# Optimization experiments

Hardware: AMD Instinct MI355X
Metric: run time of the kernel (lower is better)

Reference implementation:

```python
import jax, jax.numpy as jnp
import numpy as np

D_MODEL = 1024
D_FF = 4096
NUM_EXPERTS = 8
TOP_K = 2
BATCH = 2
SEQ = 2048


def setup_inputs() -> dict:
    key = jax.random.key(0)
    ks = jax.random.split(key, 6)
    s_in = 1.0 / np.sqrt(D_MODEL)
    s_ff = 1.0 / np.sqrt(D_FF)
    return {
        "x": jax.random.normal(ks[0], (BATCH, SEQ, D_MODEL), dtype=jnp.float32),
        "gate_w": jax.random.normal(ks[1], (D_MODEL, NUM_EXPERTS), dtype=jnp.float32) * s_in,
        "w1": jax.random.normal(ks[2], (NUM_EXPERTS, D_MODEL, D_FF), dtype=jnp.float32) * s_in,
        "b1": jnp.zeros((NUM_EXPERTS, D_FF), dtype=jnp.float32),
        "w2": jax.random.normal(ks[3], (NUM_EXPERTS, D_FF, D_MODEL), dtype=jnp.float32) * s_ff,
        "b2": jnp.zeros((NUM_EXPERTS, D_MODEL), dtype=jnp.float32),
    }


def reference(x, gate_w, w1, b1, w2, b2):
    B, S, D = x.shape
    T = B * S
    # Router: logits -> softmax -> top-k -> renormalize selected weights
    router_logits = jnp.einsum("bsd,de->bse", x, gate_w)  # [B,S,E]
    probs = jax.nn.softmax(router_logits, axis=-1)
    top_k_weights, top_k_indices = jax.lax.top_k(probs, TOP_K)  # [B,S,K]
    top_k_weights = top_k_weights / jnp.sum(top_k_weights, axis=-1, keepdims=True)

    x_flat = x.reshape(T, D)
    # per-token, per-expert combine weight: sum over k of weight * (idx==e) -> [T,E]
    one_hot = jax.nn.one_hot(top_k_indices.reshape(T, TOP_K), NUM_EXPERTS, dtype=x.dtype)
    combine = jnp.einsum("tke,tk->te", one_hot, top_k_weights.reshape(T, TOP_K))

    # Dense grouped-GEMM over all experts (same math as masked gather/scatter loop,
    # since combine weight is zero for unselected experts)
    h = jnp.maximum(jnp.einsum("td,edf->etf", x_flat, w1) + b1[:, None, :], 0.0)  # [E,T,F]
    y = jnp.einsum("etf,efd->etd", h, w2) + b2[:, None, :]  # [E,T,D]
    out_flat = jnp.einsum("etd,te->td", y, combine)  # [T,D]
    output = out_flat.reshape(B, S, D)
    return output, router_logits, top_k_indices, top_k_weights
```

## Files before the change

kernel.cpp:

```cpp
#include <hip/hip_runtime.h>
#include <cstdint>
#include <cstddef>


#define D_MODEL 1024
#define D_FF    4096
#define NEXP    8
#define TOKENS  4096
#define SLOTS   8192
#define SLOTSP  9216

typedef __bf16 bf16x8 __attribute__((ext_vector_type(8)));
typedef float  f32x4  __attribute__((ext_vector_type(4)));

static __device__ __forceinline__ unsigned short f2bf(float f) {
  unsigned int u = __float_as_uint(f);
  u += 0x7fffu + ((u >> 16) & 1u);
  return (unsigned short)(u >> 16);
}

static __device__ __forceinline__ void async_ld16(const void* g, void* l) {
  __builtin_amdgcn_global_load_lds(
      (const __attribute__((address_space(1))) void*)g,
      (__attribute__((address_space(3))) void*)l, 16, 0, 0);
}


__global__ void init_kernel(int* __restrict__ tok_list) {
  const int g = blockIdx.x * 256 + threadIdx.x;
  if (g < SLOTSP) tok_list[g] = -1;
}

__global__ __launch_bounds__(256) void router_kernel(
    const float* __restrict__ x, const float* __restrict__ gw,
    float* __restrict__ out_logits, float* __restrict__ out_idx,
    float* __restrict__ out_w)
{
  const int w = threadIdx.x >> 6, lane = threadIdx.x & 63;
  const int t = blockIdx.x * 4 + w;
  float p[NEXP];
#pragma unroll
  for (int e = 0; e < NEXP; ++e) p[e] = 0.f;
  const float* xr = x + (size_t)t * D_MODEL;
#pragma unroll 4
  for (int i = 0; i < D_MODEL / 64; ++i) {
    const int d = i * 64 + lane;
    const float xv = xr[d];
    const float* g = gw + (size_t)d * NEXP;
#pragma unroll
    for (int e = 0; e < NEXP; ++e) p[e] += xv * g[e];
  }
#pragma unroll
  for (int e = 0; e < NEXP; ++e) {
#pragma unroll
    for (int s = 1; s < 64; s <<= 1) p[e] += __shfl_xor(p[e], s, 64);
  }
  if (lane == 0) {
    int i0 = 0;
#pragma unroll
    for (int e = 1; e < NEXP; ++e) if (p[e] > p[i0]) i0 = e;
    int i1 = (i0 == 0) ? 1 : 0;
#pragma unroll
    for (int e = 0; e < NEXP; ++e)
      if (e != i0 && p[e] > p[i1]) i1 = e;
    const float w0 = 1.f / (1.f + __expf(p[i1] - p[i0]));
#pragma unroll
    for (int e = 0; e < NEXP; ++e) out_logits[(size_t)t * NEXP + e] = p[e];
    out_idx[t * 2 + 0] = (float)i0;
    out_idx[t * 2 + 1] = (float)i1;
    out_w[t * 2 + 0] = w0;
    out_w[t * 2 + 1] = 1.f - w0;
  }
}

__global__ __launch_bounds__(256) void count_offsets_kernel(
    const float* __restrict__ out_idx, int* __restrict__ wsI)
{
  __shared__ int hist[NEXP];
  const int tid = threadIdx.x;
  if (tid < NEXP) hist[tid] = 0;
  if (tid < NEXP) wsI[8 + tid] = 0;
  __syncthreads();
  int c[NEXP];
#pragma unroll
  for (int e = 0; e < NEXP; ++e) c[e] = 0;
  for (int p = tid * 32; p < tid * 32 + 32; ++p) c[(int)out_idx[p]]++;
#pragma unroll
  for (int e = 0; e < NEXP; ++e) if (c[e]) atomicAdd(&hist[e], c[e]);
  __syncthreads();
  if (tid == 0) {
    int s = 0, nb = 0;
    for (int e = 0; e < NEXP; ++e) {
      wsI[16 + e] = s;
      const int nblk = (hist[e] + 127) >> 7;
      for (int j = 0; j < nblk; ++j) {
        wsI[32 + nb] = e;
        wsI[128 + nb] = s + j * 128;
        ++nb;
      }
      s += nblk << 7;
    }
    wsI[16 + NEXP] = s;
    wsI[25] = nb;
  }
}

__global__ void scatter_kernel(const float* __restrict__ out_idx,
                               int* __restrict__ cursor,
                               const int* __restrict__ po,
                               int* __restrict__ pair_slot,
                               int* __restrict__ tok_list)
{
  const int p = blockIdx.x * 256 + threadIdx.x;
  const int lane = threadIdx.x & 63;
  const int e = (int)out_idx[p];
  int pos = 0;
#pragma unroll
  for (int e8 = 0; e8 < NEXP; ++e8) {
    const unsigned long long m = __ballot(e == e8);
    if (m) {
      const int leader = __ffsll((long long)m) - 1;
      int base = 0;
      if (lane == leader) base = atomicAdd(&cursor[e8], (int)__popcll(m));
      base = __shfl(base, leader, 64);
      if (e == e8)
        pos = po[e8] + base +
              (int)__popcll(m & ((1ull << lane) - 1ull));
    }
  }
  tok_list[pos] = p >> 1;
  pair_slot[p] = pos;
}

__global__ __launch_bounds__(256) void gather_cvt(
    const float* __restrict__ x, const int* __restrict__ tok_list,
    unsigned short* __restrict__ xg)
{
  const int gid = blockIdx.x * 256 + threadIdx.x;
  const int row = gid >> 7, seg = gid & 127;
  const int tok = tok_list[row];
  if (tok < 0) return;
  const float* src = x + (size_t)tok * D_MODEL + seg * 8;
  const float4 a = *(const float4*)(src);
  const float4 b = *(const float4*)(src + 4);
  ushort4 lo = make_ushort4(f2bf(a.x), f2bf(a.y), f2bf(a.z), f2bf(a.w));
  ushort4 hi = make_ushort4(f2bf(b.x), f2bf(b.y), f2bf(b.z), f2bf(b.w));
  unsigned short* d = xg + (size_t)row * D_MODEL + seg * 8;
  *(ushort4*)(d) = lo;
  *(ushort4*)(d + 4) = hi;
}

__global__ __launch_bounds__(256) void transpose_cvt(
    const float* __restrict__ src, unsigned short* __restrict__ dst,
    int K, int N)
{
  const int e = blockIdx.z;
  const int n0 = blockIdx.x * 64;
  const int k0 = blockIdx.y * 64;
  __shared__ float t[64][65];
  const int c4 = (threadIdx.x & 15) * 4;
  const int r  = threadIdx.x >> 4;
  const float* s = src + (size_t)e * K * N + (size_t)k0 * N + n0;
#pragma unroll
  for (int i = 0; i < 4; ++i) {
    const float4 v = *(const float4*)(s + (size_t)(r + 16 * i) * N + c4);
    t[r + 16 * i][c4 + 0] = v.x;
    t[r + 16 * i][c4 + 1] = v.y;
    t[r + 16 * i][c4 + 2] = v.z;
    t[r + 16 * i][c4 + 3] = v.w;
  }
  __syncthreads();
  unsigned short* d = dst + (size_t)e * N * K + (size_t)n0 * K + k0;
#pragma unroll
  for (int i = 0; i < 4; ++i) {
    const int n = r + 16 * i;
    ushort4 v;
    v.x = f2bf(t[c4 + 0][n]);
    v.y = f2bf(t[c4 + 1][n]);
    v.z = f2bf(t[c4 + 2][n]);
    v.w = f2bf(t[c4 + 3][n]);
    *(ushort4*)(d + (size_t)n * K + c4) = v;
  }
}

template <int RELU>
__global__ __launch_bounds__(256) void gemm_mfma(
    const unsigned short* __restrict__ A, const unsigned short* __restrict__ Bt,
    const float* __restrict__ bias, void* __restrict__ Cout,
    const int* __restrict__ wsI, int K, int N)
{
  const int gx = gridDim.x;
  const int nwg = gx * gridDim.y;
  const int cpx = nwg >> 3;
  int f = blockIdx.y * gx + blockIdx.x;
  f = (f & 7) * cpx + (f >> 3);
  const int bx = f % gx;
  const int by = f / gx;

  if (by >= wsI[25]) return;
  const int e   = wsI[32 + by];
  const int gr0 = wsI[128 + by];
  const int col0 = bx * 128;

  __shared__ unsigned short ldsA[2][128 * 64];
  __shared__ unsigned short ldsB[2][128 * 64];

  const int tid = threadIdx.x;
  const int lane = tid & 63;
  const int w = tid >> 6;
  const int wr = w >> 1, wc = w & 1;
  const int m15 = lane & 15, q = lane >> 4;

  f32x4 zero = {0.f, 0.f, 0.f, 0.f};
  f32x4 acc[4][4];
#pragma unroll
  for (int mt = 0; mt < 4; ++mt)
#pragma unroll
    for (int nt = 0; nt < 4; ++nt) acc[mt][nt] = zero;

  const size_t off0 = (size_t)(tid >> 3) * K + ((tid & 7) ^ ((tid >> 3) & 7)) * 8;
  const size_t jstep = (size_t)32 * K;
  const unsigned short* Abase = A + (size_t)gr0 * K;
  const unsigned short* Bbase = Bt + (size_t)e * N * K + (size_t)col0 * K;

  const int sw = q ^ (m15 & 7);

  auto stage = [&](int buf, int kk) {
#pragma unroll
    for (int j = 0; j < 4; ++j) {
      async_ld16(Abase + off0 + j * jstep + kk, &ldsA[buf][(j * 256 + tid) * 8]);
      async_ld16(Bbase + off0 + j * jstep + kk, &ldsB[buf][(j * 256 + tid) * 8]);
    }
  };

  stage(0, 0);
  __syncthreads();

  int cur = 0;
  for (int kk = 0; kk < K; kk += 64) {
    if (kk + 64 < K) stage(cur ^ 1, kk + 64);
#pragma unroll
    for (int ks2 = 0; ks2 < 2; ++ks2) {
      const int slot8 = (sw ^ (ks2 << 2)) * 8;
      bf16x8 af[4], bf[4];
#pragma unroll
      for (int mt = 0; mt < 4; ++mt)
        af[mt] = *(const bf16x8*)&ldsA[cur][(wr * 64 + mt * 16 + m15) * 64 + slot8];
#pragma unroll
      for (int nt = 0; nt < 4; ++nt)
        bf[nt] = *(const bf16x8*)&ldsB[cur][(wc * 64 + nt * 16 + m15) * 64 + slot8];
      __builtin_amdgcn_s_setprio(1);
#pragma unroll
      for (int mt = 0; mt < 4; ++mt)
#pragma unroll
        for (int nt = 0; nt < 4; ++nt)
          acc[mt][nt] = __builtin_amdgcn_mfma_f32_16x16x32_bf16(
              af[mt], bf[nt], acc[mt][nt], 0, 0, 0);
      __builtin_amdgcn_s_setprio(0);
    }
    __syncthreads();
    cur ^= 1;
  }

#pragma unroll
  for (int nt = 0; nt < 4; ++nt) {
    const int c = col0 + wc * 64 + nt * 16 + m15;
    const float bv = bias[(size_t)e * N + c];
#pragma unroll
    for (int mt = 0; mt < 4; ++mt) {
      const size_t rbase = (size_t)(gr0 + wr * 64 + mt * 16 + q * 4);
      if (RELU) {
        unsigned short* Cp = (unsigned short*)Cout;
#pragma unroll
        for (int i = 0; i < 4; ++i)
          Cp[(rbase + i) * N + c] = f2bf(fmaxf(acc[mt][nt][i] + bv, 0.f));
      } else {
        float* Cp = (float*)Cout;
#pragma unroll
        for (int i = 0; i < 4; ++i)
          Cp[(rbase + i) * N + c] = acc[mt][nt][i] + bv;
      }
    }
  }
}

__global__ __launch_bounds__(256) void combine_kernel(
    const float* __restrict__ y, const int* __restrict__ pair_slot,
    const float* __restrict__ out_w, float* __restrict__ out)
{
  const int gid = blockIdx.x * 256 + threadIdx.x;
  if (gid >= TOKENS * (D_MODEL / 4)) return;
  const int t = gid >> 8;
  const int qd = gid & 255;
  const float w0 = out_w[t * 2 + 0], w1 = out_w[t * 2 + 1];
  const int p0 = pair_slot[t * 2 + 0], p1 = pair_slot[t * 2 + 1];
  const float4 a = *(const float4*)(y + (size_t)p0 * D_MODEL + qd * 4);
  const float4 b = *(const float4*)(y + (size_t)p1 * D_MODEL + qd * 4);
  float4 o;
  o.x = w0 * a.x + w1 * b.x;
  o.y = w0 * a.y + w1 * b.y;
  o.z = w0 * a.z + w1 * b.z;
  o.w = w0 * a.w + w1 * b.w;
  *(float4*)(out + (size_t)t * D_MODEL + qd * 4) = o;
}

extern "C" void kernel_launch(void* const* d_in, const int* in_sizes, int n_in,
                              void* d_out, int out_size, void* d_ws, size_t ws_size,
                              hipStream_t stream)
{
  (void)in_sizes; (void)n_in; (void)out_size; (void)ws_size;
  const float* x  = (const float*)d_in[0];
  const float* gw = (const float*)d_in[1];
  const float* w1 = (const float*)d_in[2];
  const float* b1 = (const float*)d_in[3];
  const float* w2 = (const float*)d_in[4];
  const float* b2 = (const float*)d_in[5];

  float* out        = (float*)d_out;
  float* out_logits = out + (size_t)TOKENS * D_MODEL;
  float* out_idx    = out_logits + (size_t)TOKENS * NEXP;
  float* out_w      = out_idx + (size_t)TOKENS * 2;

  int* wsI       = (int*)d_ws;
  int* po        = wsI + 16;
  int* tok_list  = wsI + 512;
  int* pair_slot = wsI + 10240;
  unsigned short* xg  = (unsigned short*)((char*)d_ws + (1 << 17));
  unsigned short* w1t = xg  + (size_t)SLOTSP * D_MODEL;
  unsigned short* w2t = w1t + (size_t)NEXP * D_FF * D_MODEL;
  unsigned short* h   = w2t + (size_t)NEXP * D_MODEL * D_FF;
  float*          y   = (float*)(h + (size_t)SLOTSP * D_FF);

  init_kernel<<<SLOTSP / 256, 256, 0, stream>>>(tok_list);
  router_kernel<<<TOKENS / 4, 256, 0, stream>>>(x, gw, out_logits, out_idx, out_w);
  count_offsets_kernel<<<1, 256, 0, stream>>>(out_idx, wsI);
  scatter_kernel<<<SLOTS / 256, 256, 0, stream>>>(out_idx, wsI + 8, po, pair_slot, tok_list);
  gather_cvt<<<SLOTSP * 128 / 256, 256, 0, stream>>>(x, tok_list, xg);
  transpose_cvt<<<dim3(D_FF / 64, D_MODEL / 64, NEXP), 256, 0, stream>>>(w1, w1t, D_MODEL, D_FF);
  transpose_cvt<<<dim3(D_MODEL / 64, D_FF / 64, NEXP), 256, 0, stream>>>(w2, w2t, D_FF, D_MODEL);
  gemm_mfma<1><<<dim3(D_FF / 128, 72, 1), 256, 0, stream>>>(
      xg, w1t, b1, (void*)h, wsI, D_MODEL, D_FF);
  gemm_mfma<0><<<dim3(D_MODEL / 128, 72, 1), 256, 0, stream>>>(
      h, w2t, b2, (void*)y, wsI, D_FF, D_MODEL);
  combine_kernel<<<(TOKENS * D_MODEL / 4) / 256, 256, 0, stream>>>(
      y, pair_slot, out_w, out);
}
```

Before: 655.5 us.

## Split-K the second expert GEMM and drop LDS double buffering

Launches the down-projection GEMM with two K-slices, so the grid has twice as many blocks. Each slice writes its own fp32 partial output, and the combine kernel sums the two partials while it applies the routing weights. The GEMM kernel now stages through a single LDS buffer with load-sync-compute-sync steps and no longer uses s_setprio. Halving LDS per block may allow more resident blocks, but load/compute overlap inside each block is lost, and this also affects the first GEMM. The partial-output buffer reuses the workspace of the already-consumed gathered activations and transposed W1, and combine must now read twice as much data.

```diff
diff --git a/kernel.cpp b/kernel.cpp
--- a/kernel.cpp
+++ b/kernel.cpp
@@ -202,8 +202,12 @@
   const int gr0 = wsI[128 + by];
   const int col0 = bx * 128;
 
-  __shared__ unsigned short ldsA[2][128 * 64];
-  __shared__ unsigned short ldsB[2][128 * 64];
+  const int klen = K / gridDim.z;
+  const int kbeg = blockIdx.z * klen;
+  const int kend = kbeg + klen;
+
+  __shared__ unsigned short ldsA[128 * 64];
+  __shared__ unsigned short ldsB[128 * 64];
 
   const int tid = threadIdx.x;
   const int lane = tid & 63;
@@ -225,47 +229,38 @@
 
   const int sw = q ^ (m15 & 7);
 
-  auto stage = [&](int buf, int kk) {
+  for (int kk = kbeg; kk < kend; kk += 64) {
 #pragma unroll
     for (int j = 0; j < 4; ++j) {
-      async_ld16(Abase + off0 + j * jstep + kk, &ldsA[buf][(j * 256 + tid) * 8]);
-      async_ld16(Bbase + off0 + j * jstep + kk, &ldsB[buf][(j * 256 + tid) * 8]);
-    }
-  };
-
-  stage(0, 0);
-  __syncthreads();
-
-  int cur = 0;
-  for (int kk = 0; kk < K; kk += 64) {
-    if (kk + 64 < K) stage(cur ^ 1, kk + 64);
+      async_ld16(Abase + off0 + j * jstep + kk, &ldsA[(j * 256 + tid) * 8]);
+      async_ld16(Bbase + off0 + j * jstep + kk, &ldsB[(j * 256 + tid) * 8]);
+    }
+    __syncthreads();
 #pragma unroll
     for (int ks2 = 0; ks2 < 2; ++ks2) {
       const int slot8 = (sw ^ (ks2 << 2)) * 8;
       bf16x8 af[4], bf[4];
 #pragma unroll
       for (int mt = 0; mt < 4; ++mt)
-        af[mt] = *(const bf16x8*)&ldsA[cur][(wr * 64 + mt * 16 + m15) * 64 + slot8];
+        af[mt] = *(const bf16x8*)&ldsA[(wr * 64 + mt * 16 + m15) * 64 + slot8];
 #pragma unroll
       for (int nt = 0; nt < 4; ++nt)
-        bf[nt] = *(const bf16x8*)&ldsB[cur][(wc * 64 + nt * 16 + m15) * 64 + slot8];
-      __builtin_amdgcn_s_setprio(1);
+        bf[nt] = *(const bf16x8*)&ldsB[(wc * 64 + nt * 16 + m15) * 64 + slot8];
 #pragma unroll
       for (int mt = 0; mt < 4; ++mt)
 #pragma unroll
         for (int nt = 0; nt < 4; ++nt)
           acc[mt][nt] = __builtin_amdgcn_mfma_f32_16x16x32_bf16(
               af[mt], bf[nt], acc[mt][nt], 0, 0, 0);
-      __builtin_amdgcn_s_setprio(0);
     }
     __syncthreads();
-    cur ^= 1;
-  }
-
+  }
+
+  const size_t zoff = (size_t)blockIdx.z * SLOTSP * (size_t)N;
 #pragma unroll
   for (int nt = 0; nt < 4; ++nt) {
     const int c = col0 + wc * 64 + nt * 16 + m15;
-    const float bv = bias[(size_t)e * N + c];
+    const float bv = (blockIdx.z == 0) ? bias[(size_t)e * N + c] : 0.f;
 #pragma unroll
     for (int mt = 0; mt < 4; ++mt) {
       const size_t rbase = (size_t)(gr0 + wr * 64 + mt * 16 + q * 4);
@@ -275,7 +270,7 @@
         for (int i = 0; i < 4; ++i)
           Cp[(rbase + i) * N + c] = f2bf(fmaxf(acc[mt][nt][i] + bv, 0.f));
       } else {
-        float* Cp = (float*)Cout;
+        float* Cp = (float*)Cout + zoff;
 #pragma unroll
         for (int i = 0; i < 4; ++i)
           Cp[(rbase + i) * N + c] = acc[mt][nt][i] + bv;
@@ -294,13 +289,16 @@
   const int qd = gid & 255;
   const float w0 = out_w[t * 2 + 0], w1 = out_w[t * 2 + 1];
   const int p0 = pair_slot[t * 2 + 0], p1 = pair_slot[t * 2 + 1];
-  const float4 a = *(const float4*)(y + (size_t)p0 * D_MODEL + qd * 4);
-  const float4 b = *(const float4*)(y + (size_t)p1 * D_MODEL + qd * 4);
+  const float* y1 = y + (size_t)SLOTSP * D_MODEL;
+  const float4 a0 = *(const float4*)(y  + (size_t)p0 * D_MODEL + qd * 4);
+  const float4 a1 = *(const float4*)(y1 + (size_t)p0 * D_MODEL + qd * 4);
+  const float4 b0 = *(const float4*)(y  + (size_t)p1 * D_MODEL + qd * 4);
+  const float4 b1 = *(const float4*)(y1 + (size_t)p1 * D_MODEL + qd * 4);
   float4 o;
-  o.x = w0 * a.x + w1 * b.x;
-  o.y = w0 * a.y + w1 * b.y;
-  o.z = w0 * a.z + w1 * b.z;
-  o.w = w0 * a.w + w1 * b.w;
+  o.x = w0 * (a0.x + a1.x) + w1 * (b0.x + b1.x);
+  o.y = w0 * (a0.y + a1.y) + w1 * (b0.y + b1.y);
+  o.z = w0 * (a0.z + a1.z) + w1 * (b0.z + b1.z);
+  o.w = w0 * (a0.w + a1.w) + w1 * (b0.w + b1.w);
   *(float4*)(out + (size_t)t * D_MODEL + qd * 4) = o;
 }
 
@@ -329,7 +327,7 @@
   unsigned short* w1t = xg  + (size_t)SLOTSP * D_MODEL;
   unsigned short* w2t = w1t + (size_t)NEXP * D_FF * D_MODEL;
   unsigned short* h   = w2t + (size_t)NEXP * D_MODEL * D_FF;
-  float*          y   = (float*)(h + (size_t)SLOTSP * D_FF);
+  float*          y   = (float*)xg;
 
   init_kernel<<<SLOTSP / 256, 256, 0, stream>>>(tok_list);
   router_kernel<<<TOKENS / 4, 256, 0, stream>>>(x, gw, out_logits, out_idx, out_w);
@@ -340,7 +338,7 @@
   transpose_cvt<<<dim3(D_MODEL / 64, D_FF / 64, NEXP), 256, 0, stream>>>(w2, w2t, D_FF, D_MODEL);
   gemm_mfma<1><<<dim3(D_FF / 128, 72, 1), 256, 0, stream>>>(
       xg, w1t, b1, (void*)h, wsI, D_MODEL, D_FF);
-  gemm_mfma<0><<<dim3(D_MODEL / 128, 72, 1), 256, 0, stream>>>(
+  gemm_mfma<0><<<dim3(D_MODEL / 128, 72, 2), 256, 0, stream>>>(
       h, w2t, b2, (void*)y, wsI, D_FF, D_MODEL);
   combine_kernel<<<(TOKENS * D_MODEL / 4) / 256, 256, 0, stream>>>(
       y, pair_slot, out_w, out);
```

Result: faster. 594.8 us (-9.3%).
